# Kernel tuning notes

Measured on AMD Instinct MI355X. Metric: run time of the kernel, lower is better.

The kernel has to match this reference:

```python
import jax, jax.numpy as jnp
import numpy as np

B, N, E, D, L, NC = 48, 96, 1024, 300, 4, 7
NEG = 1e30


def _gru(x, h, w_ih, w_hh, b_ih, b_hh):
    # torch.nn.GRUCell math; weights are (3D, D) in torch layout
    gi = x @ w_ih.T + b_ih
    gh = h @ w_hh.T + b_hh
    ir, iz, inn = jnp.split(gi, 3, axis=-1)
    hr, hz, hn = jnp.split(gh, 3, axis=-1)
    r = jax.nn.sigmoid(ir + hr)
    z = jax.nn.sigmoid(iz + hz)
    n = jnp.tanh(inn + r * hn)
    return (1.0 - z) * n + z * h


def _layer(Cin, Hin, adj, cwi, cwh, cbi, cbh, pwi, pwh, pbi, pbh, wq, wk, gb):
    b, n, d = Cin.shape
    zeros = jnp.zeros((b, d), Cin.dtype)
    c0 = _gru(Cin[:, 0], zeros, cwi, cwh, cbi, cbh)          # GRUCell with h=0
    p0 = _gru(zeros, Cin[:, 0], pwi, pwh, pbi, pbh)          # M=0 at step 0
    P0 = jnp.zeros_like(Cin).at[:, 0].set(p0)                # growing P kept as full buffer
    pos = jnp.arange(n)

    def step(P, i):
        q = Cin[:, i]                                        # (B, D)
        mask = adj[:, i] * (pos < i).astype(adj.dtype)       # only predecessors j < i
        # GatLinear: Linear(cat(Q,K)) == Q.wq + K.wk + b
        alpha = (q @ wq)[:, None] + P @ wk + gb              # (B, N)
        alpha = alpha - (1.0 - mask) * NEG                   # mask_logic
        w = jax.nn.softmax(alpha, axis=-1)
        M = jnp.einsum('bn,bnd->bd', w, P)
        c_i = _gru(q, M, cwi, cwh, cbi, cbh)
        p_i = _gru(M, Hin[:, i], pwi, pwh, pbi, pbh)
        P = jax.lax.dynamic_update_slice(P, p_i[:, None, :], (0, i, 0))
        return P, c_i

    P, Cs = jax.lax.scan(step, P0, jnp.arange(1, n))
    CL = jnp.concatenate([c0[:, None], jnp.moveaxis(Cs, 0, 1)], axis=1)  # (B, N, D)
    return CL, P


def reference(features, adj, s_mask, fc1_w, fc1_b,
              gc_wih, gc_whh, gc_bih, gc_bhh,
              gp_wih, gp_whh, gp_bih, gp_bhh,
              gat_wq, gat_wk, gat_b,
              mlp_w0, mlp_b0, mlp_w1, mlp_b1, mlp_w2, mlp_b2):
    # s_mask is unused when no_rel_attn=True (faithful to torch forward)
    H0 = jax.nn.relu(features @ fc1_w + fc1_b)
    H_list = [H0]
    C_list = [H0]
    for l in range(L):
        CL, P = _layer(C_list[l], H_list[l], adj,
                       gc_wih[l], gc_whh[l], gc_bih[l], gc_bhh[l],
                       gp_wih[l], gp_whh[l], gp_bih[l], gp_bhh[l],
                       gat_wq[l], gat_wk[l], gat_b[l])
        C_list.append(CL)
        H_list.append(CL)
        H_list.append(P)
    H_list.append(features)
    H = jnp.concatenate(H_list, axis=2)                      # (B, N, 9D + E)
    x = jax.nn.relu(H @ mlp_w0 + mlp_b0)
    x = jax.nn.relu(x @ mlp_w1 + mlp_b1)
    logits = x @ mlp_w2 + mlp_b2                             # (B, N, NC)
    return logits


def setup_inputs() -> dict:
    key = jax.random.key(0)
    ks = jax.random.split(key, 25)
    s = 0.02

    def p(k, shape):
        return jax.random.normal(k, shape, jnp.float32) * s

    features = jax.random.normal(ks[0], (B, N, E), jnp.float32)
    # DAG adjacency: random predecessors, strictly lower-triangular, previous
    # utterance always connected (guarantees a nonempty attention context)
    base = jax.random.bernoulli(ks[1], 0.5, (B, N, N)).astype(jnp.float32)
    tri = jnp.tril(jnp.ones((N, N), jnp.float32), -1)
    prev = jnp.eye(N, k=-1, dtype=jnp.float32)
    adj = jnp.maximum(base * tri, prev[None])
    s_mask = jax.random.randint(ks[2], (B, N, N), 0, 2, jnp.int32)
    in_dim = D * (2 * L + 1) + E
    return {
        'features': features, 'adj': adj, 's_mask': s_mask,
        'fc1_w': p(ks[3], (E, D)), 'fc1_b': p(ks[4], (D,)),
        'gc_wih': p(ks[5], (L, 3 * D, D)), 'gc_whh': p(ks[6], (L, 3 * D, D)),
        'gc_bih': p(ks[7], (L, 3 * D)), 'gc_bhh': p(ks[8], (L, 3 * D)),
        'gp_wih': p(ks[9], (L, 3 * D, D)), 'gp_whh': p(ks[10], (L, 3 * D, D)),
        'gp_bih': p(ks[11], (L, 3 * D)), 'gp_bhh': p(ks[12], (L, 3 * D)),
        'gat_wq': p(ks[13], (L, D)), 'gat_wk': p(ks[14], (L, D)), 'gat_b': p(ks[15], (L,)),
        'mlp_w0': p(ks[16], (in_dim, D)), 'mlp_b0': p(ks[17], (D,)),
        'mlp_w1': p(ks[18], (D, D)), 'mlp_b1': p(ks[19], (D,)),
        'mlp_w2': p(ks[20], (D, NC)), 'mlp_b2': p(ks[21], (NC,)),
    }
```

## Files before the change

### kernel.cpp

```cpp
#include <hip/hip_runtime.h>
#include <math.h>

#define BB 48
#define NN 96
#define EE 1024
#define DD 300
#define LL 4
#define G3 900
#define PP 150
#define PP2 152
#define NC4 38
#define HDIM 3724
#define ROWS (BB*NN)
#define NEGI -1.0e30f
#define KP300 304
#define GIC_TILES 540

#define NPF  12
#define NLDS 5

typedef _Float16 half2_t __attribute__((ext_vector_type(2)));
typedef _Float16 h8 __attribute__((ext_vector_type(8)));
typedef float f4 __attribute__((ext_vector_type(4)));

__device__ __forceinline__ float sigm(float x){
    return __fdividef(1.0f, 1.0f + __expf(-x));
}
__device__ __forceinline__ float ftanh(float x){
    float e = __expf(2.0f*x);
    return 1.0f - __fdividef(2.0f, e + 1.0f);
}

__device__ __forceinline__ void dot4(const h8 wv, const h8 mc,
                                     float& a0, float& a1, float& a2, float& a3)
{
    half2_t w0,w1,w2,w3,m0,m1,m2,m3;
    w0.x=wv[0]; w0.y=wv[1]; m0.x=mc[0]; m0.y=mc[1];
    w1.x=wv[2]; w1.y=wv[3]; m1.x=mc[2]; m1.y=mc[3];
    w2.x=wv[4]; w2.y=wv[5]; m2.x=mc[4]; m2.y=mc[5];
    w3.x=wv[6]; w3.y=wv[7]; m3.x=mc[6]; m3.y=mc[7];
    a0 = __builtin_amdgcn_fdot2(w0, m0, a0, false);
    a1 = __builtin_amdgcn_fdot2(w1, m1, a1, false);
    a2 = __builtin_amdgcn_fdot2(w2, m2, a2, false);
    a3 = __builtin_amdgcn_fdot2(w3, m3, a3, false);
}

__global__ __launch_bounds__(256) void pack_w_q(const float* __restrict__ src_all,
                                                h8* __restrict__ dst)
{
    int l = blockIdx.y;
    int idx = blockIdx.x*256 + threadIdx.x;
    if (idx >= NC4*G3) return;
    int c = idx / G3, gate = idx % G3;
    const float* src = src_all + (size_t)l*G3*DD + (size_t)gate*DD;
    h8 v;
    #pragma unroll
    for (int j=0;j<8;j++){
        int d = 8*c + j;
        v[j] = (d<DD) ? (_Float16)src[d] : (_Float16)0.f;
    }
    dst[(size_t)l*NC4*G3 + idx] = v;
}

__global__ __launch_bounds__(256) void conv_gru_w(const float* __restrict__ gp_whh,
                                                  const float* __restrict__ gc_wih,
                                                  const float* __restrict__ gc_whh,
                                                  _Float16* __restrict__ outp)
{
    int z = blockIdx.y; int l = z/3, wsel = z%3;
    const float* src = (wsel==0?gp_whh:wsel==1?gc_wih:gc_whh) + (size_t)l*G3*DD;
    _Float16* dst = outp + (size_t)z*G3*KP300;
    int idx = blockIdx.x*256 + threadIdx.x;
    if (idx >= G3*KP300) return;
    int n = idx/KP300, k = idx%KP300;
    dst[idx] = (k<DD) ? (_Float16)src[(size_t)n*DD+k] : (_Float16)0.f;
}

__global__ __launch_bounds__(256) void convT(const float* __restrict__ src,
                                             _Float16* __restrict__ dst,
                                             int K, int N, int Kpad)
{
    int idx = blockIdx.x*256 + threadIdx.x;
    if (idx >= N*Kpad) return;
    int n = idx/Kpad, k = idx%Kpad;
    dst[idx] = (k<K) ? (_Float16)src[(size_t)k*N + n] : (_Float16)0.f;
}

__device__ __forceinline__ void gemm_tile(
    int m0, int n0, int tid,
    const float* __restrict__ A, int lda,
    const _Float16* __restrict__ B, int Kpad,
    const float* __restrict__ bias,
    float* __restrict__ C, int ldc,
    int N, int K, int relu,
    _Float16 (*As)[40], _Float16 (*Bs)[40])
{
    int w = tid>>6, lane = tid&63;
    int wy = w>>1, wx = w&1;
    int lm = lane&15, q = lane>>4;

    f4 acc[4][2];
    #pragma unroll
    for (int a=0;a<4;a++)
        #pragma unroll
        for (int b=0;b<2;b++)
            #pragma unroll
            for (int r=0;r<4;r++) acc[a][b][r]=0.f;

    int am = tid>>1, akg = (tid&1)*16;
    int bn = tid>>2, bkg = (tid&3)*8;
    const float* arow = A + (size_t)(m0+am)*lda;

    for (int k0=0; k0<K; k0+=32){
        {
            __align__(16) _Float16 av[16];
            #pragma unroll
            for (int u=0;u<16;u+=4){
                int k = k0 + akg + u;
                float x0,x1,x2,x3;
                if (k+4 <= K){
                    float4 v = *(const float4*)(arow + k);
                    x0=v.x;x1=v.y;x2=v.z;x3=v.w;
                } else {
                    x0 = (k  <K)? arow[k  ]:0.f;
                    x1 = (k+1<K)? arow[k+1]:0.f;
                    x2 = (k+2<K)? arow[k+2]:0.f;
                    x3 = (k+3<K)? arow[k+3]:0.f;
                }
                av[u]=(_Float16)x0; av[u+1]=(_Float16)x1;
                av[u+2]=(_Float16)x2; av[u+3]=(_Float16)x3;
            }
            *(h8*)&As[am][akg]   = *(h8*)&av[0];
            *(h8*)&As[am][akg+8] = *(h8*)&av[8];
        }
        {
            int gk = k0 + bkg;
            h8 bv;
            #pragma unroll
            for (int j=0;j<8;j++) bv[j]=(_Float16)0.f;
            if (n0+bn < N && gk < Kpad)
                bv = *(const h8*)(B + (size_t)(n0+bn)*Kpad + gk);
            *(h8*)&Bs[bn][bkg] = bv;
        }
        __syncthreads();
        h8 af[4], bf[2];
        #pragma unroll
        for (int mb=0; mb<4; mb++) af[mb] = *(h8*)&As[wy*64+mb*16+lm][q*8];
        #pragma unroll
        for (int nb=0; nb<2; nb++) bf[nb] = *(h8*)&Bs[wx*32+nb*16+lm][q*8];
        #pragma unroll
        for (int mb=0; mb<4; mb++)
            #pragma unroll
            for (int nb=0; nb<2; nb++)
                acc[mb][nb] = __builtin_amdgcn_mfma_f32_16x16x32_f16(af[mb], bf[nb], acc[mb][nb], 0,0,0);
        __syncthreads();
    }
    #pragma unroll
    for (int mb=0; mb<4; mb++){
        int r0 = m0 + wy*64 + mb*16 + q*4;
        #pragma unroll
        for (int nb=0; nb<2; nb++){
            int c = n0 + wx*32 + nb*16 + lm;
            if (c < N){
                float bb = bias[c];
                #pragma unroll
                for (int reg=0; reg<4; reg++){
                    float v = acc[mb][nb][reg] + bb;
                    if (relu) v = fmaxf(v, 0.f);
                    C[(size_t)(r0+reg)*ldc + c] = v;
                }
            }
        }
    }
}

__global__ __launch_bounds__(256) void gemm_mfma(
    const float* __restrict__ A, int lda,
    const _Float16* __restrict__ B, int Kpad,
    const float* __restrict__ bias,
    float* __restrict__ C, int ldc,
    int N, int K, int relu)
{
    __shared__ _Float16 As[128][40];
    __shared__ _Float16 Bs[64][40];
    gemm_tile(blockIdx.y*128, blockIdx.x*64, threadIdx.x,
              A, lda, B, Kpad, bias, C, ldc, N, K, relu, As, Bs);
}

__global__ void featcopy(const float* __restrict__ f, float* __restrict__ H)
{
    size_t row = blockIdx.x;
    int t = threadIdx.x;
    float4 v = *(const float4*)(f + row*EE + t*4);
    *(float4*)(H + row*HDIM + 2700 + t*4) = v;
}

__global__ __launch_bounds__(1024, 4) void scan_kernel(
    float* __restrict__ Hbuf,
    const float* __restrict__ GHp,
    const h8* __restrict__ pwiQ,
    const h8* __restrict__ pwhQ,
    const float* __restrict__ pbi,
    const float* __restrict__ pbh,
    const float* __restrict__ wk,
    const float* __restrict__ wq,
    const float* __restrict__ gat_b, int lidx,
    const float* __restrict__ adj,
    float* __restrict__ Mbuf,
    int ccol, int hcol, int pcol,
    const _Float16* __restrict__ cwiF,
    const float* __restrict__ cbi,
    float* __restrict__ GIc)
{
    __shared__ __align__(16) char pool[146432];

    if (blockIdx.x >= BB){
        if (threadIdx.x < 256){
            _Float16 (*As)[40] = (_Float16 (*)[40])pool;
            _Float16 (*Bs)[40] = (_Float16 (*)[40])(pool + 128*40*2);
            int bid = blockIdx.x - BB;
            int n0 = (bid % 15)*64, m0 = (bid / 15)*128;
            gemm_tile(m0, n0, threadIdx.x, Hbuf + ccol, HDIM, cwiF, KP300,
                      cbi, GIc, G3, G3, DD, 0, As, Bs);
        }
        return;
    }

    int b = blockIdx.x;
    int t = threadIdx.x;

    half2_t (*P_h2)[PP]   = (half2_t (*)[PP])(pool);
    h8*      Wlds         = (h8*)(pool + 57600);
    float*   g_s          = (float*)(pool + 129600);
    float  (*Mpart)[DD]   = (float (*)[DD])(pool + 133200);
    float*   ghp_s        = (float*)(pool + 136800);
    float*   hv_s         = (float*)(pool + 140400);
    float*   pw_s         = (float*)(pool + 141600);
    half2_t* M_h2         = (half2_t*)(pool + 142800);
    float*   e_s          = (float*)(pool + 143424);
    float*   pk_s         = (float*)(pool + 143808);
    float*   qd_s         = (float*)(pool + 144192);
    unsigned (*adjb)[4]   = (unsigned (*)[4])(pool + 144576);

    size_t rowbase = (size_t)b*NN;

    float pbi_r = (t < G3) ? pbi[t] : 0.f;
    float2 wk_r = make_float2(0.f,0.f);
    if (t < PP) wk_r = *(const float2*)&wk[2*t];

    for (int idx=t; idx<NLDS*G3; idx+=1024)
        Wlds[idx] = pwiQ[(size_t)(NPF + idx/G3)*G3 + (idx%G3)];
    if (t < NN*3){
        int r = t/3, w = t%3;
        const float* arow = adj + (rowbase + r)*NN + w*32;
        unsigned m = 0;
        for (int c=0;c<32;c++) if (arow[c] != 0.f) m |= (1u<<c);
        adjb[r][w] = m;
    }
    {
        int w = t>>6, lane = t&63;
        float gb = gat_b[lidx];
        for (int r = w; r < NN; r += 16){
            const float* x = Hbuf + (rowbase + r)*HDIM + ccol;
            float s = 0.f;
            for (int d=lane; d<DD; d+=64) s += x[d]*wq[d];
            #pragma unroll
            for (int o=32;o>0;o>>=1) s += __shfl_xor(s,o);
            if (lane==0) qd_s[r] = s + gb;
        }
    }
    if (t < PP){
        float2 c2 = *(const float2*)&Hbuf[rowbase*HDIM + ccol + 2*t];
        Mpart[0][2*t] = c2.x; Mpart[0][2*t+1] = c2.y;
        half2_t mh; mh.x = (_Float16)c2.x; mh.y = (_Float16)c2.y;
        M_h2[t] = mh;
    } else if (t < PP2){
        half2_t z; z.x=(_Float16)0.f; z.y=(_Float16)0.f;
        M_h2[t] = z;
    }
    __syncthreads();
    if (t < G3){
        const h8* W2 = pwhQ + t;
        float a0=0.f, a1=0.f, a2=0.f, a3=0.f;
        #pragma unroll 4
        for (int c=0;c<NC4;c++){
            h8 wv = W2[(size_t)c*G3];
            h8 mc = *(h8*)&M_h2[4*c];
            dot4(wv, mc, a0,a1,a2,a3);
        }
        g_s[t] = pbh[t] + (a0+a2) + (a1+a3);
    }
    __syncthreads();
    if (t < PP){
        int d0 = 2*t, d1 = 2*t+1;
        float r0  = sigm(pbi[d0]      + g_s[d0]);
        float z0  = sigm(pbi[DD+d0]   + g_s[DD+d0]);
        float n0  = ftanh(pbi[2*DD+d0] + r0*g_s[2*DD+d0]);
        float p0  = (1.f-z0)*n0 + z0*Mpart[0][d0];
        float r1  = sigm(pbi[d1]      + g_s[d1]);
        float z1  = sigm(pbi[DD+d1]   + g_s[DD+d1]);
        float n1  = ftanh(pbi[2*DD+d1] + r1*g_s[2*DD+d1]);
        float p1  = (1.f-z1)*n1 + z1*Mpart[0][d1];
        *(float2*)&Hbuf[rowbase*HDIM + pcol + d0] = make_float2(p0,p1);
        half2_t ph; ph.x = (_Float16)p0; ph.y = (_Float16)p1;
        P_h2[0][t] = ph;
        pw_s[d0] = p0*wk_r.x;
        pw_s[d1] = p1*wk_r.y;
        *(float2*)&Mbuf[rowbase*DD + d0] = make_float2(0.f,0.f);
    }
    __syncthreads();

    for (int i=1;i<NN;i++){
        size_t row = rowbase + i;

        h8 pf0,pf1,pf2,pf3,pf4,pf5,pf6,pf7,pf8,pf9,pf10,pf11;
        if (t < G3){
            const h8* W = pwiQ + t;
            pf0 = W[0];             pf1 = W[(size_t)1*G3];  pf2 = W[(size_t)2*G3];
            pf3 = W[(size_t)3*G3];  pf4 = W[(size_t)4*G3];  pf5 = W[(size_t)5*G3];
            pf6 = W[(size_t)6*G3];  pf7 = W[(size_t)7*G3];  pf8 = W[(size_t)8*G3];
            pf9 = W[(size_t)9*G3];  pf10 = W[(size_t)10*G3]; pf11 = W[(size_t)11*G3];
            asm volatile("" : "+v"(pf0),"+v"(pf1),"+v"(pf2),"+v"(pf3),"+v"(pf4),"+v"(pf5));
            asm volatile("" : "+v"(pf6),"+v"(pf7),"+v"(pf8),"+v"(pf9),"+v"(pf10),"+v"(pf11));
        }

        if (t < 64){
            float s = 0.f;
            for (int c=t;c<DD;c+=64) s += pw_s[c];
            #pragma unroll
            for (int o=32;o>0;o>>=1) s += __shfl_xor(s,o);
            if (t==0) pk_s[i-1] = s;
            float q = qd_s[i];
            float a0 = NEGI, a1 = NEGI;
            if (t < i){
                if ((adjb[i][t>>5]>>(t&31))&1u) a0 = q + ((t==i-1)? s : pk_s[t]);
            }
            int j1 = 64+t;
            if (t < 32 && j1 < i){
                if ((adjb[i][2]>>t)&1u) a1 = q + ((j1==i-1)? s : pk_s[j1]);
            }
            float m = fmaxf(a0,a1);
            #pragma unroll
            for (int o=32;o>0;o>>=1) m = fmaxf(m, __shfl_xor(m,o));
            float e0 = __expf(a0-m);
            float e1 = (t<32)? __expf(a1-m) : 0.f;
            float ss = e0+e1;
            #pragma unroll
            for (int o=32;o>0;o>>=1) ss += __shfl_xor(ss,o);
            float inv = __fdividef(1.f, ss);
            e_s[t] = e0*inv;
            if (t<32) e_s[64+t] = e1*inv;
        }
        __syncthreads();
        if (t < 450){
            int g = t/150, dp = t%150;
            int cnt = (i+2)/3;
            int j0 = g*cnt; int j1 = j0+cnt; if (j1 > i) j1 = i;
            float m0=0.f, m1=0.f;
            for (int j=j0;j<j1;j++){
                float w = e_s[j];
                half2_t pv = P_h2[j][dp];
                m0 += w*(float)pv.x;
                m1 += w*(float)pv.y;
            }
            *(float2*)&Mpart[g][2*dp] = make_float2(m0,m1);
        } else if (t >= 512){
            int k = t-512;
            #pragma unroll
            for (int it=0; it<2; it++){
                int idx = k + it*512;
                if (idx < 450){
                    *(float2*)&ghp_s[2*idx] = *(const float2*)&GHp[row*G3 + 2*idx];
                } else if (idx < 600){
                    int h = idx-450;
                    *(float2*)&hv_s[2*h] = *(const float2*)&Hbuf[row*HDIM + hcol + 2*h];
                }
            }
        }
        __syncthreads();
        if (t < PP){
            float m0 = Mpart[0][2*t] + Mpart[1][2*t] + Mpart[2][2*t];
            float m1 = Mpart[0][2*t+1] + Mpart[1][2*t+1] + Mpart[2][2*t+1];
            half2_t mh; mh.x = (_Float16)m0; mh.y = (_Float16)m1;
            M_h2[t] = mh;
            *(float2*)&Mbuf[row*DD + 2*t] = make_float2(m0,m1);
        }
        __syncthreads();
        if (t < G3){
            const h8* W = pwiQ + t;
            const h8* Mc = (const h8*)M_h2;
            float a0=0.f, a1=0.f, a2=0.f, a3=0.f;
            dot4(pf0,  Mc[0],  a0,a1,a2,a3);
            dot4(pf1,  Mc[1],  a0,a1,a2,a3);
            dot4(pf2,  Mc[2],  a0,a1,a2,a3);
            dot4(pf3,  Mc[3],  a0,a1,a2,a3);
            dot4(pf4,  Mc[4],  a0,a1,a2,a3);
            dot4(pf5,  Mc[5],  a0,a1,a2,a3);
            dot4(pf6,  Mc[6],  a0,a1,a2,a3);
            dot4(pf7,  Mc[7],  a0,a1,a2,a3);
            dot4(pf8,  Mc[8],  a0,a1,a2,a3);
            dot4(pf9,  Mc[9],  a0,a1,a2,a3);
            dot4(pf10, Mc[10], a0,a1,a2,a3);
            dot4(pf11, Mc[11], a0,a1,a2,a3);
            dot4(Wlds[t],        Mc[NPF+0], a0,a1,a2,a3);
            dot4(Wlds[G3+t],     Mc[NPF+1], a0,a1,a2,a3);
            dot4(Wlds[2*G3+t],   Mc[NPF+2], a0,a1,a2,a3);
            dot4(Wlds[3*G3+t],   Mc[NPF+3], a0,a1,a2,a3);
            dot4(Wlds[4*G3+t],   Mc[NPF+4], a0,a1,a2,a3);
            #pragma unroll 4
            for (int c=NPF+NLDS;c<NC4;c++){
                h8 wv = W[(size_t)c*G3];
                dot4(wv, Mc[c], a0,a1,a2,a3);
            }
            g_s[t] = pbi_r + (a0+a2) + (a1+a3);
        }
        __syncthreads();
        if (t < PP){
            int d0 = 2*t, d1 = 2*t+1;
            float2 hv = *(const float2*)&hv_s[d0];
            float r0  = sigm(g_s[d0]      + ghp_s[d0]);
            float z0  = sigm(g_s[DD+d0]   + ghp_s[DD+d0]);
            float n0  = ftanh(g_s[2*DD+d0] + r0*ghp_s[2*DD+d0]);
            float p0  = (1.f-z0)*n0 + z0*hv.x;
            float r1  = sigm(g_s[d1]      + ghp_s[d1]);
            float z1  = sigm(g_s[DD+d1]   + ghp_s[DD+d1]);
            float n1  = ftanh(g_s[2*DD+d1] + r1*ghp_s[2*DD+d1]);
            float p1  = (1.f-z1)*n1 + z1*hv.y;
            *(float2*)&Hbuf[row*HDIM + pcol + d0] = make_float2(p0,p1);
            half2_t ph; ph.x = (_Float16)p0; ph.y = (_Float16)p1;
            P_h2[i][t] = ph;
            pw_s[d0] = p0*wk_r.x;
            pw_s[d1] = p1*wk_r.y;
        }
        __syncthreads();
    }
}

__global__ __launch_bounds__(320) void combine_c(
    const float* __restrict__ GIc, const float* __restrict__ GHc,
    const float* __restrict__ Mbuf, float* __restrict__ Hbuf, int clcol)
{
    size_t row = blockIdx.x;
    int d = threadIdx.x;
    if (d < DD){
        float ir = GIc[row*G3+d], iz = GIc[row*G3+DD+d], inn = GIc[row*G3+2*DD+d];
        float hr = GHc[row*G3+d], hz = GHc[row*G3+DD+d], hn  = GHc[row*G3+2*DD+d];
        float r  = sigm(ir+hr);
        float z  = sigm(iz+hz);
        float nn = ftanh(inn + r*hn);
        float h  = Mbuf[row*DD+d];
        Hbuf[row*HDIM + clcol + d] = (1.f-z)*nn + z*h;
    }
}

__global__ __launch_bounds__(64) void logits_kernel(
    const float* __restrict__ x2, const float* __restrict__ w2,
    const float* __restrict__ b2, float* __restrict__ out)
{
    size_t row = blockIdx.x;
    int lane = threadIdx.x;
    float acc[7]={0,0,0,0,0,0,0};
    for (int d=lane; d<DD; d+=64){
        float x = x2[row*DD+d];
        #pragma unroll
        for (int c=0;c<7;c++) acc[c] += x*w2[d*7+c];
    }
    #pragma unroll
    for (int c=0;c<7;c++){
        float s = acc[c];
        #pragma unroll
        for (int o=32;o>0;o>>=1) s += __shfl_down(s,o);
        if (lane==0) out[row*7+c] = s + b2[c];
    }
}

extern "C" void kernel_launch(void* const* d_in, const int* in_sizes, int n_in,
                              void* d_out, int out_size, void* d_ws, size_t ws_size,
                              hipStream_t stream)
{
    const float* features = (const float*)d_in[0];
    const float* adj      = (const float*)d_in[1];
    const float* fc1_w    = (const float*)d_in[3];
    const float* fc1_b    = (const float*)d_in[4];
    const float* gc_wih   = (const float*)d_in[5];
    const float* gc_whh   = (const float*)d_in[6];
    const float* gc_bih   = (const float*)d_in[7];
    const float* gc_bhh   = (const float*)d_in[8];
    const float* gp_wih   = (const float*)d_in[9];
    const float* gp_whh   = (const float*)d_in[10];
    const float* gp_bih   = (const float*)d_in[11];
    const float* gp_bhh   = (const float*)d_in[12];
    const float* gat_wq   = (const float*)d_in[13];
    const float* gat_wk   = (const float*)d_in[14];
    const float* gat_b    = (const float*)d_in[15];
    const float* mlp_w0   = (const float*)d_in[16];
    const float* mlp_b0   = (const float*)d_in[17];
    const float* mlp_w1   = (const float*)d_in[18];
    const float* mlp_b1   = (const float*)d_in[19];
    const float* mlp_w2   = (const float*)d_in[20];
    const float* mlp_b2   = (const float*)d_in[21];
    float* out = (float*)d_out;

    float* ws = (float*)d_ws;
    size_t off = 0;
    float* Hbuf = ws + off; off += (size_t)ROWS*HDIM;
    float* bufA = ws + off; off += (size_t)ROWS*G3;
    float* bufB = ws + off; off += (size_t)ROWS*G3;
    float* bufC = ws + off; off += (size_t)ROWS*G3;
    float* Mbuf = ws + off; off += (size_t)ROWS*DD;
    h8* pwiQ = (h8*)(ws + off); off += (size_t)LL*NC4*G3*4;
    h8* pwhQ = (h8*)(ws + off); off += (size_t)LL*NC4*G3*4;
    _Float16* gruF = (_Float16*)(ws + off); off += (size_t)12*G3*KP300/2;
    _Float16* fc1F = (_Float16*)(ws + off); off += (size_t)DD*EE/2;
    _Float16* mlp0F= (_Float16*)(ws + off); off += (size_t)DD*3728/2;
    _Float16* mlp1F= (_Float16*)(ws + off); off += (size_t)DD*KP300/2;
    (void)ws_size; (void)in_sizes; (void)n_in; (void)out_size;

    {
        pack_w_q<<<dim3((NC4*G3+255)/256, LL), 256, 0, stream>>>(gp_wih, pwiQ);
        pack_w_q<<<dim3((NC4*G3+255)/256, LL), 256, 0, stream>>>(gp_whh, pwhQ);
        conv_gru_w<<<dim3((G3*KP300+255)/256, 12), 256, 0, stream>>>(gp_whh, gc_wih, gc_whh, gruF);
        convT<<<(DD*EE+255)/256, 256, 0, stream>>>(fc1_w, fc1F, EE, DD, EE);
        convT<<<(DD*3728+255)/256, 256, 0, stream>>>(mlp_w0, mlp0F, HDIM, DD, 3728);
        convT<<<(DD*KP300+255)/256, 256, 0, stream>>>(mlp_w1, mlp1F, DD, DD, KP300);
    }
    gemm_mfma<<<dim3(5,36),256,0,stream>>>(features, EE, fc1F, EE, fc1_b,
                                           Hbuf, HDIM, DD, EE, 1);
    featcopy<<<ROWS,256,0,stream>>>(features, Hbuf);

    for (int l=0;l<LL;l++){
        int ccol  = (l==0)? 0 : 300 + (l-1)*600;
        int hcol  = l*300;
        int pcol  = 600 + l*600;
        int clcol = 300 + l*600;
        const h8* pwiQl = pwiQ + (size_t)l*NC4*G3;
        const h8* pwhQl = pwhQ + (size_t)l*NC4*G3;
        const _Float16* pwhF = gruF + (size_t)(l*3+0)*G3*KP300;
        const _Float16* cwiF = gruF + (size_t)(l*3+1)*G3*KP300;
        const _Float16* cwhF = gruF + (size_t)(l*3+2)*G3*KP300;

        gemm_mfma<<<dim3(15,36),256,0,stream>>>(Hbuf+hcol, HDIM, pwhF, KP300,
                                                gp_bhh + l*G3, bufA, G3, G3, DD, 0);
        scan_kernel<<<BB+GIC_TILES,1024,0,stream>>>(Hbuf, bufA, pwiQl, pwhQl,
                                          gp_bih + l*G3, gp_bhh + l*G3,
                                          gat_wk + l*DD, gat_wq + l*DD, gat_b, l,
                                          adj, Mbuf, ccol, hcol, pcol,
                                          cwiF, gc_bih + l*G3, bufB);
        gemm_mfma<<<dim3(15,36),256,0,stream>>>(Mbuf, DD, cwhF, KP300,
                                                gc_bhh + l*G3, bufC, G3, G3, DD, 0);
        combine_c<<<ROWS,320,0,stream>>>(bufB, bufC, Mbuf, Hbuf, clcol);
    }

    gemm_mfma<<<dim3(5,36),256,0,stream>>>(Hbuf, HDIM, mlp0F, 3728, mlp_b0,
                                           bufB, DD, DD, HDIM, 1);
    gemm_mfma<<<dim3(5,36),256,0,stream>>>(bufB, DD, mlp1F, KP300, mlp_b1,
                                           bufC, DD, DD, DD, 1);
    logits_kernel<<<ROWS,64,0,stream>>>(bufC, mlp_w2, mlp_b2, out);
}
```

Measured before the change: 3.262 ms.

## Drop shift-invariant query term, use running softmax max, restage GRU weights

Removes the per-row query and bias term from the attention logits, since it is constant across keys and cancels in the softmax. The per-step max reduction is replaced by a running maximum over all key scores produced so far. The key score of each new P row is now reduced with warp shuffles by the threads that produce it, instead of a separate pass over a shared array. The register prefetch of 12 weight chunks is dropped, 6 chunks are held in LDS instead, and unroll pragmas are added. Dropping the prefetch means the remaining weight loads no longer overlap the softmax stage, and the larger LDS pool may limit occupancy.

Result: faster. 3.017 ms (-7.5%).

```diff
diff --git a/kernel.cpp b/kernel.cpp
--- a/kernel.cpp
+++ b/kernel.cpp
@@ -16,8 +16,7 @@
 #define KP300 304
 #define GIC_TILES 540
 
-#define NPF  12
-#define NLDS 5
+#define NLDS 6
 
 typedef _Float16 half2_t __attribute__((ext_vector_type(2)));
 typedef _Float16 h8 __attribute__((ext_vector_type(8)));
@@ -212,7 +211,8 @@
     const float* __restrict__ cbi,
     float* __restrict__ GIc)
 {
-    __shared__ __align__(16) char pool[146432];
+    __shared__ __align__(16) char pool[158976];
+    (void)wq; (void)gat_b; (void)lidx;
 
     if (blockIdx.x >= BB){
         if (threadIdx.x < 256){
@@ -231,16 +231,15 @@
 
     half2_t (*P_h2)[PP]   = (half2_t (*)[PP])(pool);
     h8*      Wlds         = (h8*)(pool + 57600);
-    float*   g_s          = (float*)(pool + 129600);
-    float  (*Mpart)[DD]   = (float (*)[DD])(pool + 133200);
-    float*   ghp_s        = (float*)(pool + 136800);
-    float*   hv_s         = (float*)(pool + 140400);
-    float*   pw_s         = (float*)(pool + 141600);
-    half2_t* M_h2         = (half2_t*)(pool + 142800);
-    float*   e_s          = (float*)(pool + 143424);
-    float*   pk_s         = (float*)(pool + 143808);
-    float*   qd_s         = (float*)(pool + 144192);
-    unsigned (*adjb)[4]   = (unsigned (*)[4])(pool + 144576);
+    float*   g_s          = (float*)(pool + 144000);
+    float  (*Mpart)[DD]   = (float (*)[DD])(pool + 147600);
+    float*   ghp_s        = (float*)(pool + 151200);
+    float*   hv_s         = (float*)(pool + 154800);
+    half2_t* M_h2         = (half2_t*)(pool + 156000);
+    float*   e_s          = (float*)(pool + 156640);
+    float*   pk_s         = (float*)(pool + 157024);
+    float*   pksum        = (float*)(pool + 157408);
+    unsigned (*adjb)[4]   = (unsigned (*)[4])(pool + 157440);
 
     size_t rowbase = (size_t)b*NN;
 
@@ -249,25 +248,13 @@
     if (t < PP) wk_r = *(const float2*)&wk[2*t];
 
     for (int idx=t; idx<NLDS*G3; idx+=1024)
-        Wlds[idx] = pwiQ[(size_t)(NPF + idx/G3)*G3 + (idx%G3)];
+        Wlds[idx] = pwiQ[idx];
     if (t < NN*3){
         int r = t/3, w = t%3;
         const float* arow = adj + (rowbase + r)*NN + w*32;
         unsigned m = 0;
         for (int c=0;c<32;c++) if (arow[c] != 0.f) m |= (1u<<c);
         adjb[r][w] = m;
-    }
-    {
-        int w = t>>6, lane = t&63;
-        float gb = gat_b[lidx];
-        for (int r = w; r < NN; r += 16){
-            const float* x = Hbuf + (rowbase + r)*HDIM + ccol;
-            float s = 0.f;
-            for (int d=lane; d<DD; d+=64) s += x[d]*wq[d];
-            #pragma unroll
-            for (int o=32;o>0;o>>=1) s += __shfl_xor(s,o);
-            if (lane==0) qd_s[r] = s + gb;
-        }
     }
     if (t < PP){
         float2 c2 = *(const float2*)&Hbuf[rowbase*HDIM + ccol + 2*t];
@@ -291,59 +278,48 @@
         g_s[t] = pbh[t] + (a0+a2) + (a1+a3);
     }
     __syncthreads();
-    if (t < PP){
-        int d0 = 2*t, d1 = 2*t+1;
-        float r0  = sigm(pbi[d0]      + g_s[d0]);
-        float z0  = sigm(pbi[DD+d0]   + g_s[DD+d0]);
-        float n0  = ftanh(pbi[2*DD+d0] + r0*g_s[2*DD+d0]);
-        float p0  = (1.f-z0)*n0 + z0*Mpart[0][d0];
-        float r1  = sigm(pbi[d1]      + g_s[d1]);
-        float z1  = sigm(pbi[DD+d1]   + g_s[DD+d1]);
-        float n1  = ftanh(pbi[2*DD+d1] + r1*g_s[2*DD+d1]);
-        float p1  = (1.f-z1)*n1 + z1*Mpart[0][d1];
-        *(float2*)&Hbuf[rowbase*HDIM + pcol + d0] = make_float2(p0,p1);
-        half2_t ph; ph.x = (_Float16)p0; ph.y = (_Float16)p1;
-        P_h2[0][t] = ph;
-        pw_s[d0] = p0*wk_r.x;
-        pw_s[d1] = p1*wk_r.y;
-        *(float2*)&Mbuf[rowbase*DD + d0] = make_float2(0.f,0.f);
+    if (t < 192){
+        float pw = 0.f;
+        if (t < PP){
+            int d0 = 2*t, d1 = 2*t+1;
+            float r0  = sigm(pbi[d0]      + g_s[d0]);
+            float z0  = sigm(pbi[DD+d0]   + g_s[DD+d0]);
+            float n0  = ftanh(pbi[2*DD+d0] + r0*g_s[2*DD+d0]);
+            float p0  = (1.f-z0)*n0 + z0*Mpart[0][d0];
+            float r1  = sigm(pbi[d1]      + g_s[d1]);
+            float z1  = sigm(pbi[DD+d1]   + g_s[DD+d1]);
+            float n1  = ftanh(pbi[2*DD+d1] + r1*g_s[2*DD+d1]);
+            float p1  = (1.f-z1)*n1 + z1*Mpart[0][d1];
+            *(float2*)&Hbuf[rowbase*HDIM + pcol + d0] = make_float2(p0,p1);
+            half2_t ph; ph.x = (_Float16)p0; ph.y = (_Float16)p1;
+            P_h2[0][t] = ph;
+            pw = p0*wk_r.x + p1*wk_r.y;
+            *(float2*)&Mbuf[rowbase*DD + d0] = make_float2(0.f,0.f);
+        }
+        #pragma unroll
+        for (int o=32;o>0;o>>=1) pw += __shfl_xor(pw,o);
+        if ((t&63)==0) pksum[t>>6] = pw;
     }
     __syncthreads();
+
+    float m_run = NEGI;
 
     for (int i=1;i<NN;i++){
         size_t row = rowbase + i;
-
-        h8 pf0,pf1,pf2,pf3,pf4,pf5,pf6,pf7,pf8,pf9,pf10,pf11;
-        if (t < G3){
-            const h8* W = pwiQ + t;
-            pf0 = W[0];             pf1 = W[(size_t)1*G3];  pf2 = W[(size_t)2*G3];
-            pf3 = W[(size_t)3*G3];  pf4 = W[(size_t)4*G3];  pf5 = W[(size_t)5*G3];
-            pf6 = W[(size_t)6*G3];  pf7 = W[(size_t)7*G3];  pf8 = W[(size_t)8*G3];
-            pf9 = W[(size_t)9*G3];  pf10 = W[(size_t)10*G3]; pf11 = W[(size_t)11*G3];
-            asm volatile("" : "+v"(pf0),"+v"(pf1),"+v"(pf2),"+v"(pf3),"+v"(pf4),"+v"(pf5));
-            asm volatile("" : "+v"(pf6),"+v"(pf7),"+v"(pf8),"+v"(pf9),"+v"(pf10),"+v"(pf11));
-        }
-
         if (t < 64){
-            float s = 0.f;
-            for (int c=t;c<DD;c+=64) s += pw_s[c];
-            #pragma unroll
-            for (int o=32;o>0;o>>=1) s += __shfl_xor(s,o);
-            if (t==0) pk_s[i-1] = s;
-            float q = qd_s[i];
+            float s_last = pksum[0]+pksum[1]+pksum[2];
+            if (t==0) pk_s[i-1] = s_last;
+            m_run = fmaxf(m_run, s_last);
             float a0 = NEGI, a1 = NEGI;
             if (t < i){
-                if ((adjb[i][t>>5]>>(t&31))&1u) a0 = q + ((t==i-1)? s : pk_s[t]);
+                if ((adjb[i][t>>5]>>(t&31))&1u) a0 = (t==i-1)? s_last : pk_s[t];
             }
             int j1 = 64+t;
             if (t < 32 && j1 < i){
-                if ((adjb[i][2]>>t)&1u) a1 = q + ((j1==i-1)? s : pk_s[j1]);
-            }
-            float m = fmaxf(a0,a1);
-            #pragma unroll
-            for (int o=32;o>0;o>>=1) m = fmaxf(m, __shfl_xor(m,o));
-            float e0 = __expf(a0-m);
-            float e1 = (t<32)? __expf(a1-m) : 0.f;
+                if ((adjb[i][2]>>t)&1u) a1 = (j1==i-1)? s_last : pk_s[j1];
+            }
+            float e0 = __expf(a0 - m_run);
+            float e1 = (t<32)? __expf(a1 - m_run) : 0.f;
             float ss = e0+e1;
             #pragma unroll
             for (int o=32;o>0;o>>=1) ss += __shfl_xor(ss,o);
@@ -357,6 +333,7 @@
             int cnt = (i+2)/3;
             int j0 = g*cnt; int j1 = j0+cnt; if (j1 > i) j1 = i;
             float m0=0.f, m1=0.f;
+            #pragma unroll 4
             for (int j=j0;j<j1;j++){
                 float w = e_s[j];
                 half2_t pv = P_h2[j][dp];
@@ -390,47 +367,41 @@
             const h8* W = pwiQ + t;
             const h8* Mc = (const h8*)M_h2;
             float a0=0.f, a1=0.f, a2=0.f, a3=0.f;
-            dot4(pf0,  Mc[0],  a0,a1,a2,a3);
-            dot4(pf1,  Mc[1],  a0,a1,a2,a3);
-            dot4(pf2,  Mc[2],  a0,a1,a2,a3);
-            dot4(pf3,  Mc[3],  a0,a1,a2,a3);
-            dot4(pf4,  Mc[4],  a0,a1,a2,a3);
-            dot4(pf5,  Mc[5],  a0,a1,a2,a3);
-            dot4(pf6,  Mc[6],  a0,a1,a2,a3);
-            dot4(pf7,  Mc[7],  a0,a1,a2,a3);
-            dot4(pf8,  Mc[8],  a0,a1,a2,a3);
-            dot4(pf9,  Mc[9],  a0,a1,a2,a3);
-            dot4(pf10, Mc[10], a0,a1,a2,a3);
-            dot4(pf11, Mc[11], a0,a1,a2,a3);
-            dot4(Wlds[t],        Mc[NPF+0], a0,a1,a2,a3);
-            dot4(Wlds[G3+t],     Mc[NPF+1], a0,a1,a2,a3);
-            dot4(Wlds[2*G3+t],   Mc[NPF+2], a0,a1,a2,a3);
-            dot4(Wlds[3*G3+t],   Mc[NPF+3], a0,a1,a2,a3);
-            dot4(Wlds[4*G3+t],   Mc[NPF+4], a0,a1,a2,a3);
-            #pragma unroll 4
-            for (int c=NPF+NLDS;c<NC4;c++){
+            dot4(Wlds[t],        Mc[0], a0,a1,a2,a3);
+            dot4(Wlds[G3+t],     Mc[1], a0,a1,a2,a3);
+            dot4(Wlds[2*G3+t],   Mc[2], a0,a1,a2,a3);
+            dot4(Wlds[3*G3+t],   Mc[3], a0,a1,a2,a3);
+            dot4(Wlds[4*G3+t],   Mc[4], a0,a1,a2,a3);
+            dot4(Wlds[5*G3+t],   Mc[5], a0,a1,a2,a3);
+            #pragma unroll 8
+            for (int c=NLDS;c<NC4;c++){
                 h8 wv = W[(size_t)c*G3];
                 dot4(wv, Mc[c], a0,a1,a2,a3);
             }
             g_s[t] = pbi_r + (a0+a2) + (a1+a3);
         }
         __syncthreads();
-        if (t < PP){
-            int d0 = 2*t, d1 = 2*t+1;
-            float2 hv = *(const float2*)&hv_s[d0];
-            float r0  = sigm(g_s[d0]      + ghp_s[d0]);
-            float z0  = sigm(g_s[DD+d0]   + ghp_s[DD+d0]);
-            float n0  = ftanh(g_s[2*DD+d0] + r0*ghp_s[2*DD+d0]);
-            float p0  = (1.f-z0)*n0 + z0*hv.x;
-            float r1  = sigm(g_s[d1]      + ghp_s[d1]);
-            float z1  = sigm(g_s[DD+d1]   + ghp_s[DD+d1]);
-            float n1  = ftanh(g_s[2*DD+d1] + r1*ghp_s[2*DD+d1]);
-            float p1  = (1.f-z1)*n1 + z1*hv.y;
-            *(float2*)&Hbuf[row*HDIM + pcol + d0] = make_float2(p0,p1);
-            half2_t ph; ph.x = (_Float16)p0; ph.y = (_Float16)p1;
-            P_h2[i][t] = ph;
-            pw_s[d0] = p0*wk_r.x;
-            pw_s[d1] = p1*wk_r.y;
+        if (t < 192){
+            float pw = 0.f;
+            if (t < PP){
+                int d0 = 2*t, d1 = 2*t+1;
+                float2 hv = *(const float2*)&hv_s[d0];
+                float r0  = sigm(g_s[d0]      + ghp_s[d0]);
+                float z0  = sigm(g_s[DD+d0]   + ghp_s[DD+d0]);
+                float n0  = ftanh(g_s[2*DD+d0] + r0*ghp_s[2*DD+d0]);
+                float p0  = (1.f-z0)*n0 + z0*hv.x;
+                float r1  = sigm(g_s[d1]      + ghp_s[d1]);
+                float z1  = sigm(g_s[DD+d1]   + ghp_s[DD+d1]);
+                float n1  = ftanh(g_s[2*DD+d1] + r1*ghp_s[2*DD+d1]);
+                float p1  = (1.f-z1)*n1 + z1*hv.y;
+                *(float2*)&Hbuf[row*HDIM + pcol + d0] = make_float2(p0,p1);
+                half2_t ph; ph.x = (_Float16)p0; ph.y = (_Float16)p1;
+                P_h2[i][t] = ph;
+                pw = p0*wk_r.x + p1*wk_r.y;
+            }
+            #pragma unroll
+            for (int o=32;o>0;o>>=1) pw += __shfl_xor(pw,o);
+            if ((t&63)==0) pksum[t>>6] = pw;
         }
         __syncthreads();
     }
```
